# Kernel tuning notes

Measured on AMD Instinct MI355X. Metric: run time of the kernel, lower is better.

Reference implementation:

```python
import jax, jax.numpy as jnp
import numpy as np

TOP_K = 8
N_EXPERTS = 64
ALPHA = 0.01

def setup_inputs() -> dict:
    key = jax.random.key(0)
    k1, k2 = jax.random.split(key)
    hidden_states = jax.random.normal(k1, (8, 4096, 1024), dtype=jnp.float32)
    weight = jax.random.normal(k2, (N_EXPERTS, 1024), dtype=jnp.float32) * 0.02
    return {"hidden_states": hidden_states, "weight": weight}

def reference(hidden_states, weight):
    bsz, seq_len, h = hidden_states.shape
    tokens = hidden_states.reshape(-1, h).astype(jnp.float32)          # [T, h]
    logits = tokens @ weight.astype(jnp.float32).T                     # [T, E]
    scores = jax.nn.softmax(logits, axis=-1)                           # [T, E]
    topk_weights, topk_indices = jax.lax.top_k(scores, TOP_K)          # [T, K]
    topk_indices = jnp.clip(topk_indices, 0, N_EXPERTS - 1)
    # renormalize top-k probabilities (norm_topk_prob=True, top_k>1)
    denom = topk_weights.sum(axis=-1, keepdims=True) + 1e-20
    topk_weights = topk_weights / denom
    # expert usage counts (bincount / scatter path)
    expert_counts = jnp.zeros((N_EXPERTS,), jnp.int32).at[topk_indices.reshape(-1)].add(1)
    # sequence aux loss (training path, seq_aux=True)
    idx_b = topk_indices.reshape(bsz, seq_len * TOP_K)                 # [B, S*K]
    ce = jnp.zeros((bsz, N_EXPERTS), jnp.float32)
    ce = ce.at[jnp.arange(bsz)[:, None], idx_b].add(1.0)
    ce = ce * (N_EXPERTS / (seq_len * TOP_K))
    scores_seq = scores.reshape(bsz, seq_len, N_EXPERTS)
    aux_loss = ((ce * scores_seq.mean(axis=1)).sum(axis=1)).mean() * ALPHA
    return (topk_indices.astype(jnp.int32),
            topk_weights.astype(hidden_states.dtype),
            aux_loss,
            expert_counts)
```

## Files before the change

### kernel.cpp

```cpp
#include <hip/hip_runtime.h>

#define NTOK 32768
#define HDIM 1024
#define NEXP 64
#define TK   8
#define NB   8
#define SEQ  4096

#define MB   64
#define KC   64
#define NCH  (HDIM / KC)
#define NTHR 128

typedef __attribute__((ext_vector_type(8))) short bf16x8;
typedef __attribute__((ext_vector_type(4))) float f32x4;

union BF8 { bf16x8 v; unsigned u[4]; };

__device__ inline unsigned f2bf(float x) {
    unsigned u = __float_as_uint(x);
    return (u + 0x7FFFu + ((u >> 16) & 1u)) >> 16;
}

__device__ inline void split4(float4 v, unsigned* hp, unsigned* lp) {
    unsigned h0 = f2bf(v.x), h1 = f2bf(v.y), h2 = f2bf(v.z), h3 = f2bf(v.w);
    unsigned l0 = f2bf(v.x - __uint_as_float(h0 << 16));
    unsigned l1 = f2bf(v.y - __uint_as_float(h1 << 16));
    unsigned l2 = f2bf(v.z - __uint_as_float(h2 << 16));
    unsigned l3 = f2bf(v.w - __uint_as_float(h3 << 16));
    hp[0] = h0 | (h1 << 16); hp[1] = h2 | (h3 << 16);
    lp[0] = l0 | (l1 << 16); lp[1] = l2 | (l3 << 16);
}

__device__ __forceinline__ void gl16(const void* g, void* l) {
    __builtin_amdgcn_global_load_lds(
        (const __attribute__((address_space(1))) void*)g,
        (__attribute__((address_space(3))) void*)l, 16, 0, 0);
}

__global__ void wsplit(const float* __restrict__ w,
                       unsigned short* __restrict__ whi,
                       unsigned short* __restrict__ wlo)
{
    int T = blockIdx.x * 256 + threadIdx.x;
    int slot = T >> 6, l = T & 63;
    int c = slot >> 3, s = (slot >> 2) & 1, n = slot & 3;
    int e = n * 16 + (l & 15);
    int k = c * 64 + s * 32 + (l >> 4) * 8;
    const float* src = w + (size_t)e * HDIM + k;
    float4 v0 = *(const float4*)(src);
    float4 v1 = *(const float4*)(src + 4);
    unsigned hp[4], lp[4];
    split4(v0, &hp[0], &lp[0]);
    split4(v1, &hp[2], &lp[2]);
    ((uint4*)whi)[T] = make_uint4(hp[0], hp[1], hp[2], hp[3]);
    ((uint4*)wlo)[T] = make_uint4(lp[0], lp[1], lp[2], lp[3]);
}

__global__ __launch_bounds__(NTHR, 2) void moe_main(
    const float* __restrict__ hidden,
    const unsigned short* __restrict__ w2hi,
    const unsigned short* __restrict__ w2lo,
    float* __restrict__ out,
    float* __restrict__ ws)
{
    __shared__ __align__(16) unsigned char smem[32768];
    float* sLog = (float*)smem;
    __shared__ float mxArr[MB];
    __shared__ float smSum[NEXP];
    __shared__ int   hist[NEXP];

    const int tid   = threadIdx.x;
    const int w     = tid >> 6;
    const int l     = tid & 63;
    const int m     = l & 15;
    const int q     = l >> 4;
    const int t0    = blockIdx.x * MB;
    const int wbase = tid & 64;

    if (tid < NEXP) { smSum[tid] = 0.f; hist[tid] = 0; }

    f32x4 acc[2][4];
#pragma unroll
    for (int mt = 0; mt < 2; ++mt)
#pragma unroll
        for (int n = 0; n < 4; ++n) acc[mt][n] = (f32x4)0.f;

#pragma unroll
    for (int i = 0; i < 8; ++i) {
        int slot = i * NTHR + tid;
        int r = slot >> 4, p = slot & 15, b = p ^ (r & 15);
        gl16(hidden + (size_t)(t0 + r) * HDIM + b * 4,
             smem + (size_t)(i * NTHR + wbase) * 16);
    }
    __syncthreads();

    for (int c = 0; c < NCH; ++c) {
        const unsigned char* Ab = smem + (c & 1) * 16384;

        bf16x8 bh[2][4], bl[2][4];
#pragma unroll
        for (int s = 0; s < 2; ++s)
#pragma unroll
            for (int n = 0; n < 4; ++n) {
                size_t off = ((size_t)(c * 8 + s * 4 + n) * 64 + l) * 8;
                bh[s][n] = *(const bf16x8*)(w2hi + off);
                bl[s][n] = *(const bf16x8*)(w2lo + off);
            }

        if (c + 1 < NCH) {
            unsigned char* nb = smem + ((c + 1) & 1) * 16384;
            const int kc = (c + 1) * KC;
#pragma unroll
            for (int i = 0; i < 8; ++i) {
                int slot = i * NTHR + tid;
                int r = slot >> 4, p = slot & 15, b = p ^ (r & 15);
                gl16(hidden + (size_t)(t0 + r) * HDIM + kc + b * 4,
                     nb + (size_t)(i * NTHR + wbase) * 16);
            }
        }

#pragma unroll
        for (int s = 0; s < 2; ++s) {
            BF8 ah[2], al[2];
#pragma unroll
            for (int mt = 0; mt < 2; ++mt) {
                int r = w * 32 + mt * 16 + m;
                int b0 = s * 8 + q * 2;
                int p0 = b0 ^ (r & 15), p1 = (b0 + 1) ^ (r & 15);
                float4 a0 = *(const float4*)(Ab + ((size_t)r * 16 + p0) * 16);
                float4 a1 = *(const float4*)(Ab + ((size_t)r * 16 + p1) * 16);
                split4(a0, &ah[mt].u[0], &al[mt].u[0]);
                split4(a1, &ah[mt].u[2], &al[mt].u[2]);
            }
#pragma unroll
            for (int n = 0; n < 4; ++n)
#pragma unroll
                for (int mt = 0; mt < 2; ++mt) {
                    acc[mt][n] = __builtin_amdgcn_mfma_f32_16x16x32_bf16(ah[mt].v, bh[s][n], acc[mt][n], 0, 0, 0);
                    acc[mt][n] = __builtin_amdgcn_mfma_f32_16x16x32_bf16(al[mt].v, bh[s][n], acc[mt][n], 0, 0, 0);
                    acc[mt][n] = __builtin_amdgcn_mfma_f32_16x16x32_bf16(ah[mt].v, bl[s][n], acc[mt][n], 0, 0, 0);
                }
        }
        __syncthreads();
    }

#pragma unroll
    for (int mt = 0; mt < 2; ++mt)
#pragma unroll
        for (int n = 0; n < 4; ++n)
#pragma unroll
            for (int r = 0; r < 4; ++r)
                sLog[(w * 32 + mt * 16 + q * 4 + r) * 66 + n * 16 + m] = acc[mt][n][r];
    __syncthreads();

    float regSm = 0.f;
    for (int j = 0; j < 32; ++j) {
        int t = w * 32 + j;
        float x = sLog[t * 66 + l];
        float mx = x;
#pragma unroll
        for (int off = 32; off; off >>= 1) mx = fmaxf(mx, __shfl_xor(mx, off));
        float p = __expf(x - mx);
        float sd = p;
#pragma unroll
        for (int off = 32; off; off >>= 1) sd += __shfl_xor(sd, off);
        regSm += p / sd;
        if (l == 0) mxArr[t] = mx;
    }
    atomicAdd(&smSum[l], regSm);
    __syncthreads();

    if (w == 0) {
        const float mx = mxArr[l];
        unsigned long long s8[TK];
#pragma unroll
        for (int j = 0; j < TK; ++j) s8[j] = 0ull;
        for (int e = 0; e < NEXP; ++e) {
            float x = sLog[l * 66 + e];
            unsigned u = __float_as_uint(x);
            unsigned k32 = (u & 0x80000000u) ? ~u : (u | 0x80000000u);
            unsigned long long key = ((unsigned long long)k32 << 6)
                                   | (unsigned long long)(63 - e);
            if (key > s8[TK - 1]) {
#pragma unroll
                for (int j = 0; j < TK; ++j) {
                    unsigned long long hi = s8[j] > key ? s8[j] : key;
                    key = s8[j] > key ? key : s8[j];
                    s8[j] = hi;
                }
            }
        }
        float ev[TK]; int ei[TK]; float sum = 0.f;
#pragma unroll
        for (int j = 0; j < TK; ++j) {
            unsigned k32 = (unsigned)(s8[j] >> 6);
            unsigned u = (k32 >> 31) ? (k32 ^ 0x80000000u) : ~k32;
            ev[j] = __expf(__uint_as_float(u) - mx);
            sum += ev[j];
            ei[j] = 63 - (int)(s8[j] & 63ull);
        }
        int t = t0 + l;
        float4 i0 = make_float4((float)ei[0], (float)ei[1], (float)ei[2], (float)ei[3]);
        float4 i1 = make_float4((float)ei[4], (float)ei[5], (float)ei[6], (float)ei[7]);
        *(float4*)(out + (size_t)t * TK)     = i0;
        *(float4*)(out + (size_t)t * TK + 4) = i1;
        float rs = 1.f / (sum + 1e-20f);
        float4 w0 = make_float4(ev[0] * rs, ev[1] * rs, ev[2] * rs, ev[3] * rs);
        float4 w1 = make_float4(ev[4] * rs, ev[5] * rs, ev[6] * rs, ev[7] * rs);
        *(float4*)(out + (size_t)NTOK * TK + (size_t)t * TK)     = w0;
        *(float4*)(out + (size_t)NTOK * TK + (size_t)t * TK + 4) = w1;
#pragma unroll
        for (int j = 0; j < TK; ++j) atomicAdd(&hist[ei[j]], 1);
    }
    __syncthreads();

    if (tid < NEXP) {
        int b = blockIdx.x >> 6;
        atomicAdd(&ws[b * NEXP + tid], (float)hist[tid]);
        atomicAdd(&ws[NB * NEXP + b * NEXP + tid], smSum[tid]);
    }
}

__global__ void moe_finalize(const float* __restrict__ ws, float* __restrict__ out)
{
    int e = threadIdx.x;
    float cnt = 0.f, accv = 0.f;
#pragma unroll
    for (int b = 0; b < NB; ++b) {
        float c  = ws[b * NEXP + e];
        float sm = ws[NB * NEXP + b * NEXP + e];
        cnt += c;
        accv += c * sm;
    }
    out[(size_t)NTOK * TK * 2 + 1 + e] = cnt;
#pragma unroll
    for (int off = 32; off; off >>= 1) accv += __shfl_xor(accv, off);
    if (e == 0) {
        float aux = 0.01f * accv * ((float)NEXP / ((float)SEQ * (float)TK))
                    / (float)SEQ / (float)NB;
        out[(size_t)NTOK * TK * 2] = aux;
    }
}

extern "C" void kernel_launch(void* const* d_in, const int* in_sizes, int n_in,
                              void* d_out, int out_size, void* d_ws, size_t ws_size,
                              hipStream_t stream)
{
    const float* hidden = (const float*)d_in[0];
    const float* weight = (const float*)d_in[1];
    float* out  = (float*)d_out;
    float* wsf  = (float*)d_ws;
    unsigned short* w2hi = (unsigned short*)(wsf + 2 * NB * NEXP);
    unsigned short* w2lo = w2hi + NEXP * HDIM;

    hipMemsetAsync(d_ws, 0, 2 * NB * NEXP * sizeof(float), stream);
    wsplit<<<32, 256, 0, stream>>>(weight, w2hi, w2lo);
    moe_main<<<NTOK / MB, NTHR, 0, stream>>>(hidden, w2hi, w2lo, out, wsf);
    moe_finalize<<<1, 64, 0, stream>>>(wsf, out);
}
```

Before: 238.1 us.

## Split each 64-token block across eight waves with a 4x2 wave tiling

Raises the block size from 128 to 512 threads and assigns each wave a 16-token by 32-expert sub-tile instead of a 32x64 tile. Staging loads, MFMA accumulators, the logit store and the softmax loop are all re-indexed for the 4x2 wave grid. The goal is more resident waves to hide the latency of global loads, split conversion and MFMA. The cost is that each A fragment is now split twice, B weight fragments are loaded redundantly by four waves, and register pressure rises under the tighter launch bound.

```diff
diff --git a/kernel.cpp b/kernel.cpp
--- a/kernel.cpp
+++ b/kernel.cpp
@@ -10,7 +10,7 @@
 #define MB   64
 #define KC   64
 #define NCH  (HDIM / KC)
-#define NTHR 128
+#define NTHR 512
 
 typedef __attribute__((ext_vector_type(8))) short bf16x8;
 typedef __attribute__((ext_vector_type(4))) float f32x4;
@@ -57,7 +57,7 @@
     ((uint4*)wlo)[T] = make_uint4(lp[0], lp[1], lp[2], lp[3]);
 }
 
-__global__ __launch_bounds__(NTHR, 2) void moe_main(
+__global__ __launch_bounds__(NTHR, 4) void moe_main(
     const float* __restrict__ hidden,
     const unsigned short* __restrict__ w2hi,
     const unsigned short* __restrict__ w2lo,
@@ -75,19 +75,19 @@
     const int l     = tid & 63;
     const int m     = l & 15;
     const int q     = l >> 4;
+    const int wm    = w >> 1;
+    const int wn    = w & 1;
     const int t0    = blockIdx.x * MB;
-    const int wbase = tid & 64;
+    const int wbase = tid & 448;
 
     if (tid < NEXP) { smSum[tid] = 0.f; hist[tid] = 0; }
 
-    f32x4 acc[2][4];
-#pragma unroll
-    for (int mt = 0; mt < 2; ++mt)
-#pragma unroll
-        for (int n = 0; n < 4; ++n) acc[mt][n] = (f32x4)0.f;
-
-#pragma unroll
-    for (int i = 0; i < 8; ++i) {
+    f32x4 acc[2];
+#pragma unroll
+    for (int n = 0; n < 2; ++n) acc[n] = (f32x4)0.f;
+
+#pragma unroll
+    for (int i = 0; i < 2; ++i) {
         int slot = i * NTHR + tid;
         int r = slot >> 4, p = slot & 15, b = p ^ (r & 15);
         gl16(hidden + (size_t)(t0 + r) * HDIM + b * 4,
@@ -98,12 +98,12 @@
     for (int c = 0; c < NCH; ++c) {
         const unsigned char* Ab = smem + (c & 1) * 16384;
 
-        bf16x8 bh[2][4], bl[2][4];
+        bf16x8 bh[2][2], bl[2][2];
 #pragma unroll
         for (int s = 0; s < 2; ++s)
 #pragma unroll
-            for (int n = 0; n < 4; ++n) {
-                size_t off = ((size_t)(c * 8 + s * 4 + n) * 64 + l) * 8;
+            for (int n = 0; n < 2; ++n) {
+                size_t off = ((size_t)(c * 8 + s * 4 + wn * 2 + n) * 64 + l) * 8;
                 bh[s][n] = *(const bf16x8*)(w2hi + off);
                 bl[s][n] = *(const bf16x8*)(w2lo + off);
             }
@@ -112,7 +112,7 @@
             unsigned char* nb = smem + ((c + 1) & 1) * 16384;
             const int kc = (c + 1) * KC;
 #pragma unroll
-            for (int i = 0; i < 8; ++i) {
+            for (int i = 0; i < 2; ++i) {
                 int slot = i * NTHR + tid;
                 int r = slot >> 4, p = slot & 15, b = p ^ (r & 15);
                 gl16(hidden + (size_t)(t0 + r) * HDIM + kc + b * 4,
@@ -122,41 +122,34 @@
 
 #pragma unroll
         for (int s = 0; s < 2; ++s) {
-            BF8 ah[2], al[2];
-#pragma unroll
-            for (int mt = 0; mt < 2; ++mt) {
-                int r = w * 32 + mt * 16 + m;
-                int b0 = s * 8 + q * 2;
-                int p0 = b0 ^ (r & 15), p1 = (b0 + 1) ^ (r & 15);
-                float4 a0 = *(const float4*)(Ab + ((size_t)r * 16 + p0) * 16);
-                float4 a1 = *(const float4*)(Ab + ((size_t)r * 16 + p1) * 16);
-                split4(a0, &ah[mt].u[0], &al[mt].u[0]);
-                split4(a1, &ah[mt].u[2], &al[mt].u[2]);
-            }
-#pragma unroll
-            for (int n = 0; n < 4; ++n)
-#pragma unroll
-                for (int mt = 0; mt < 2; ++mt) {
-                    acc[mt][n] = __builtin_amdgcn_mfma_f32_16x16x32_bf16(ah[mt].v, bh[s][n], acc[mt][n], 0, 0, 0);
-                    acc[mt][n] = __builtin_amdgcn_mfma_f32_16x16x32_bf16(al[mt].v, bh[s][n], acc[mt][n], 0, 0, 0);
-                    acc[mt][n] = __builtin_amdgcn_mfma_f32_16x16x32_bf16(ah[mt].v, bl[s][n], acc[mt][n], 0, 0, 0);
-                }
+            const int r  = wm * 16 + m;
+            const int b0 = s * 8 + q * 2;
+            const int p0 = b0 ^ m, p1 = (b0 + 1) ^ m;
+            float4 a0 = *(const float4*)(Ab + ((size_t)r * 16 + p0) * 16);
+            float4 a1 = *(const float4*)(Ab + ((size_t)r * 16 + p1) * 16);
+            BF8 ah, al;
+            split4(a0, &ah.u[0], &al.u[0]);
+            split4(a1, &ah.u[2], &al.u[2]);
+#pragma unroll
+            for (int n = 0; n < 2; ++n) {
+                acc[n] = __builtin_amdgcn_mfma_f32_16x16x32_bf16(ah.v, bh[s][n], acc[n], 0, 0, 0);
+                acc[n] = __builtin_amdgcn_mfma_f32_16x16x32_bf16(al.v, bh[s][n], acc[n], 0, 0, 0);
+                acc[n] = __builtin_amdgcn_mfma_f32_16x16x32_bf16(ah.v, bl[s][n], acc[n], 0, 0, 0);
+            }
         }
         __syncthreads();
     }
 
 #pragma unroll
-    for (int mt = 0; mt < 2; ++mt)
-#pragma unroll
-        for (int n = 0; n < 4; ++n)
-#pragma unroll
-            for (int r = 0; r < 4; ++r)
-                sLog[(w * 32 + mt * 16 + q * 4 + r) * 66 + n * 16 + m] = acc[mt][n][r];
+    for (int n = 0; n < 2; ++n)
+#pragma unroll
+        for (int r = 0; r < 4; ++r)
+            sLog[(wm * 16 + q * 4 + r) * 66 + (wn * 2 + n) * 16 + m] = acc[n][r];
     __syncthreads();
 
     float regSm = 0.f;
-    for (int j = 0; j < 32; ++j) {
-        int t = w * 32 + j;
+    for (int j = 0; j < 8; ++j) {
+        int t = w * 8 + j;
         float x = sLog[t * 66 + l];
         float mx = x;
 #pragma unroll
```

Result: faster. 231.8 us (-2.7%).
